# Optimization experiments

Hardware: AMD Instinct MI355X
Metric: run time of the kernel (lower is better)

The kernel has to match this reference:

```python
import jax, jax.numpy as jnp
import numpy as np

MAX_PATH_DISTANCE = 5


def setup_inputs() -> dict:
    key = jax.random.key(0)
    k1, k2, k3, k4, k5 = jax.random.split(key, 5)
    N = 8192
    E = 4_000_000
    x = jax.random.normal(k1, (N, 128), dtype=jnp.float32)
    src = jax.random.randint(k2, (E,), 0, N, dtype=jnp.int64)
    dst = jax.random.randint(k3, (E,), 0, N, dtype=jnp.int64)
    # path lengths; original computes len(paths[src][dst]) >= 1
    path_len = jax.random.randint(k4, (E,), 0, 6, dtype=jnp.int64)
    # learned parameter b of shape [max_path_distance]
    b = jax.random.normal(k5, (MAX_PATH_DISTANCE,), dtype=jnp.float32)
    return {"x": x, "b": b, "src": src, "dst": dst, "path_len": path_len}


def reference(x, b, src, dst, path_len):
    N = x.shape[0]
    # index = min(len, max_path_distance) - 1, clamped to valid range
    idx = jnp.clip(path_len, 1, MAX_PATH_DISTANCE) - 1  # [E]
    vals = b[idx]  # [E] gather from tiny table
    spatial = jnp.zeros((N, N), dtype=b.dtype)
    spatial = spatial.at[src, dst].set(vals)  # scatter into pairwise bias matrix
    return spatial
```

## Files before the change

kernel.cpp:

```cpp
#include <hip/hip_runtime.h>

#define MAX_PATH_DISTANCE 5
#define NROW 8192
#define ROWS_PER_BKT 128
#define NBKT 64
#define SLICES 17
#define EPB 4096
#define CAPB (SLICES * EPB)
#define CAPR 768
#define BLK 256
#define NWAVE 4


__device__ __forceinline__ int clamp_bidx(int pl) {
    int c = pl < 1 ? 1 : (pl > MAX_PATH_DISTANCE ? MAX_PATH_DISTANCE : pl);
    return c - 1;
}

__global__ __launch_bounds__(BLK) void se_coarse(
        const int4* __restrict__ src4, const int4* __restrict__ dst4,
        const int4* __restrict__ plen4,
        unsigned long long* __restrict__ bkt,
        unsigned int* __restrict__ bkt_cur, int E4) {
    __shared__ unsigned long long stage[EPB];
    __shared__ unsigned int hist[NWAVE][NBKT], wbase[NWAVE][NBKT];
    __shared__ unsigned int base_l[NBKT], gbase[NBKT], s_total;
    const int tid = threadIdx.x;
    const int w   = tid >> 6;
    const int q0  = blockIdx.x * (EPB / 4);

    for (int i = tid; i < NWAVE * NBKT; i += BLK)
        ((unsigned int*)hist)[i] = 0u;
    __syncthreads();

    unsigned long long ent[16];
#pragma unroll
    for (int g = 0; g < 4; ++g) {
        int q = q0 + g * BLK + tid;
        if (q < E4) {
            int4 s = src4[q], d = dst4[q], p = plen4[q];
            int ss[4] = {s.x, s.y, s.z, s.w};
            int dd[4] = {d.x, d.y, d.z, d.w};
            int pp[4] = {p.x, p.y, p.z, p.w};
#pragma unroll
            for (int c = 0; c < 4; ++c) {
                int e = q * 4 + c;
                unsigned int key = ((unsigned int)(e + 1) << 3)
                                 | (unsigned int)clamp_bidx(pp[c]);
                unsigned long long v =
                      ((unsigned long long)(unsigned int)ss[c] << 38)
                    | ((unsigned long long)(unsigned int)dd[c] << 25)
                    | (unsigned long long)key;
                ent[g * 4 + c] = v;
                atomicAdd(&hist[w][(unsigned int)(v >> 45)], 1u);
            }
        } else {
#pragma unroll
            for (int c = 0; c < 4; ++c) ent[g * 4 + c] = 0ull;
        }
    }
    __syncthreads();

    if (tid < NBKT)
        base_l[tid] = hist[0][tid] + hist[1][tid] + hist[2][tid] + hist[3][tid];
    __syncthreads();
    if (tid == 0) {
        unsigned int run = 0;
        for (int i = 0; i < NBKT; ++i) {
            unsigned int t = base_l[i]; base_l[i] = run; run += t;
        }
        s_total = run;
    }
    __syncthreads();
    if (tid < NBKT) {
        unsigned int t = base_l[tid];
        unsigned int tot = 0;
#pragma unroll
        for (int ww = 0; ww < NWAVE; ++ww) {
            wbase[ww][tid] = t; t += hist[ww][tid]; tot += hist[ww][tid];
        }
        gbase[tid] = atomicAdd(&bkt_cur[tid], tot);
    }
    __syncthreads();

#pragma unroll
    for (int j = 0; j < 16; ++j) {
        if (ent[j]) {
            unsigned int bb = (unsigned int)(ent[j] >> 45);
            unsigned int p  = atomicAdd(&wbase[w][bb], 1u);
            stage[p] = ent[j];
        }
    }
    __syncthreads();

    const unsigned int total = s_total;
    for (unsigned int i = tid; i < total; i += BLK) {
        unsigned long long v = stage[i];
        unsigned int bb  = (unsigned int)(v >> 45);
        unsigned int pos = gbase[bb] + (i - base_l[bb]);
        if (pos < CAPB) bkt[(size_t)bb * CAPB + pos] = v;
    }
}

__global__ __launch_bounds__(BLK) void se_fine(
        const unsigned long long* __restrict__ bkt,
        const unsigned int* __restrict__ bkt_cur,
        unsigned long long* __restrict__ rbins,
        unsigned int* __restrict__ rcur) {
    __shared__ unsigned long long stage[EPB];
    __shared__ unsigned int hist[NWAVE][ROWS_PER_BKT], wbase[NWAVE][ROWS_PER_BKT];
    __shared__ unsigned int base_l[ROWS_PER_BKT], gbase[ROWS_PER_BKT], s_total;
    const int tid = threadIdx.x;
    const int w   = tid >> 6;
    const int b   = blockIdx.x / SLICES;
    const int sl  = blockIdx.x % SLICES;

    unsigned int cnt = bkt_cur[b]; if (cnt > CAPB) cnt = CAPB;
    const int i0 = sl * EPB;
    int n = (int)cnt - i0;
    if (n <= 0) return;
    if (n > EPB) n = EPB;

    for (int i = tid; i < NWAVE * ROWS_PER_BKT; i += BLK)
        ((unsigned int*)hist)[i] = 0u;
    __syncthreads();

    const unsigned long long* bp = bkt + (size_t)b * CAPB + i0;
    unsigned long long ent[16];
#pragma unroll
    for (int j = 0; j < 16; ++j) {
        int i = j * BLK + tid;
        ent[j] = 0ull;
        if (i < n) {
            unsigned long long v = bp[i];
            ent[j] = v;
            atomicAdd(&hist[w][(unsigned int)(v >> 38) & 127u], 1u);
        }
    }
    __syncthreads();

    if (tid < ROWS_PER_BKT)
        base_l[tid] = hist[0][tid] + hist[1][tid] + hist[2][tid] + hist[3][tid];
    __syncthreads();
    if (tid == 0) {
        unsigned int run = 0;
        for (int i = 0; i < ROWS_PER_BKT; ++i) {
            unsigned int t = base_l[i]; base_l[i] = run; run += t;
        }
        s_total = run;
    }
    __syncthreads();
    if (tid < ROWS_PER_BKT) {
        unsigned int t = base_l[tid];
        unsigned int tot = 0;
#pragma unroll
        for (int ww = 0; ww < NWAVE; ++ww) {
            wbase[ww][tid] = t; t += hist[ww][tid]; tot += hist[ww][tid];
        }
        gbase[tid] = atomicAdd(&rcur[b * ROWS_PER_BKT + tid], tot);
    }
    __syncthreads();

#pragma unroll
    for (int j = 0; j < 16; ++j) {
        if (ent[j]) {
            unsigned int rl = (unsigned int)(ent[j] >> 38) & 127u;
            unsigned int p  = atomicAdd(&wbase[w][rl], 1u);
            stage[p] = ent[j];
        }
    }
    __syncthreads();

    const unsigned int total = s_total;
    for (unsigned int i = tid; i < total; i += BLK) {
        unsigned long long v = stage[i];
        unsigned int s   = (unsigned int)((v >> 38) & 0x1FFFu);
        unsigned int rl  = s & 127u;
        unsigned int pos = gbase[rl] + (i - base_l[rl]);
        if (pos < CAPR) rbins[(size_t)s * CAPR + pos] = v;
    }
}

__global__ __launch_bounds__(BLK) void se_rows(
        const unsigned long long* __restrict__ rbins,
        const unsigned int* __restrict__ rcur,
        const float* __restrict__ b,
        float* __restrict__ out) {
    __shared__ unsigned int lds[NROW];
    const int r = blockIdx.x, tid = threadIdx.x;

    for (int i = tid; i < NROW; i += BLK) lds[i] = 0u;

    unsigned int cnt = rcur[r]; if (cnt > CAPR) cnt = CAPR;
    const unsigned long long* bp = rbins + (size_t)r * CAPR;

    unsigned long long ev[3];
    int ne = 0;
    for (unsigned int i = tid; i < cnt; i += BLK) ev[ne++] = bp[i];
    __syncthreads();

    for (int k = 0; k < ne; ++k) {
        unsigned long long v = ev[k];
        atomicMax(&lds[(unsigned int)((v >> 25) & 0x1FFFu)],
                  (unsigned int)(v & 0x1FFFFFFu));
    }
    __syncthreads();

    for (int k = 0; k < ne; ++k) {
        unsigned long long v = ev[k];
        unsigned int key = (unsigned int)(v & 0x1FFFFFFu);
        unsigned int d   = (unsigned int)((v >> 25) & 0x1FFFu);
        if (lds[d] == key) lds[d] = __float_as_uint(b[key & 7u]);
    }
    __syncthreads();

    float4* out4 = reinterpret_cast<float4*>(out + (size_t)r * NROW);
    const float4* l4 = reinterpret_cast<const float4*>(lds);
    for (int k = tid; k < NROW / 4; k += BLK) out4[k] = l4[k];
}


__global__ void se_scatter_keys(const int* __restrict__ src,
                                const int* __restrict__ dst,
                                const int* __restrict__ plen,
                                unsigned int* __restrict__ out,
                                int E, int N) {
    int e = blockIdx.x * blockDim.x + threadIdx.x;
    if (e >= E) return;
    unsigned int key = ((unsigned int)(e + 1) << 3)
                     | (unsigned int)clamp_bidx(plen[e]);
    atomicMax(&out[(size_t)src[e] * (size_t)N + (size_t)dst[e]], key);
}

__global__ void se_resolve(const int* __restrict__ src,
                           const int* __restrict__ dst,
                           const int* __restrict__ plen,
                           const float* __restrict__ b,
                           unsigned int* __restrict__ out,
                           int E, int N) {
    int e = blockIdx.x * blockDim.x + threadIdx.x;
    if (e >= E) return;
    unsigned int key = ((unsigned int)(e + 1) << 3)
                     | (unsigned int)clamp_bidx(plen[e]);
    size_t off = (size_t)src[e] * (size_t)N + (size_t)dst[e];
    if (out[off] == key) {
        reinterpret_cast<float*>(out)[off] = b[key & 7u];
    }
}


extern "C" void kernel_launch(void* const* d_in, const int* in_sizes, int n_in,
                              void* d_out, int out_size, void* d_ws, size_t ws_size,
                              hipStream_t stream) {
    const float* b    = (const float*)d_in[1];
    const int*   src  = (const int*)d_in[2];
    const int*   dst  = (const int*)d_in[3];
    const int*   plen = (const int*)d_in[4];

    const int N = in_sizes[0] / 128;
    const int E = in_sizes[2];

    const size_t rbins_bytes = (size_t)NROW * CAPR * sizeof(unsigned long long);
    const size_t bkt_bytes   = (size_t)NBKT * CAPB * sizeof(unsigned long long);
    const size_t rcur_bytes  = (size_t)NROW * sizeof(unsigned int);
    const size_t bcur_bytes  = (size_t)NBKT * sizeof(unsigned int);
    const size_t need = rbins_bytes + bkt_bytes + rcur_bytes + bcur_bytes;

    const int block = 256;
    const int gridE = (E + block - 1) / block;

    if (N == NROW && (unsigned int)E < (1u << 22) && (E % 4) == 0 &&
        ws_size >= need) {
        unsigned long long* rbins = (unsigned long long*)d_ws;
        unsigned long long* bktp  = (unsigned long long*)((char*)d_ws + rbins_bytes);
        unsigned int* rcur  = (unsigned int*)((char*)d_ws + rbins_bytes + bkt_bytes);

        hipMemsetAsync(rcur, 0, rcur_bytes + bcur_bytes, stream);
        unsigned int* bcur = rcur + NROW;
        se_coarse<<<(E + EPB - 1) / EPB, BLK, 0, stream>>>(
            (const int4*)src, (const int4*)dst, (const int4*)plen,
            bktp, bcur, E / 4);
        se_fine<<<NBKT * SLICES, BLK, 0, stream>>>(bktp, bcur, rbins, rcur);
        se_rows<<<NROW, BLK, 0, stream>>>(rbins, rcur, b, (float*)d_out);
    } else {
        hipMemsetAsync(d_out, 0, (size_t)out_size * sizeof(float), stream);
        se_scatter_keys<<<gridE, block, 0, stream>>>(src, dst, plen,
                                                     (unsigned int*)d_out, E, N);
        se_resolve<<<gridE, block, 0, stream>>>(src, dst, plen, b,
                                                (unsigned int*)d_out, E, N);
    }
}
```

Measured before the change: 118.0 us.

## Fuse coarse, fine and row passes into one persistent cooperative kernel

Merges the memset and the three bucketing kernels into a single cooperative persistent kernel, using grid-wide syncs between phases and grid-stride task loops. The goal is to remove launch gaps and the separate memset. SLICES drops to 16 so slice indexing becomes shifts and masks, which lowers per-bucket capacity and risks overflow for skewed buckets. In exchange, occupancy is limited by the persistent grid, and grid syncs plus the occupancy/device-property queries run on every call.

```diff
diff --git a/kernel.cpp b/kernel.cpp
--- a/kernel.cpp
+++ b/kernel.cpp
@@ -1,10 +1,13 @@
 #include <hip/hip_runtime.h>
+#include <hip/hip_cooperative_groups.h>
+
+namespace cg = cooperative_groups;
 
 #define MAX_PATH_DISTANCE 5
 #define NROW 8192
 #define ROWS_PER_BKT 128
 #define NBKT 64
-#define SLICES 17
+#define SLICES 16
 #define EPB 4096
 #define CAPB (SLICES * EPB)
 #define CAPR 768
@@ -17,206 +20,206 @@
     return c - 1;
 }
 
-__global__ __launch_bounds__(BLK) void se_coarse(
+__global__ __launch_bounds__(BLK) void se_fused(
         const int4* __restrict__ src4, const int4* __restrict__ dst4,
-        const int4* __restrict__ plen4,
+        const int4* __restrict__ plen4, const float* __restrict__ b,
         unsigned long long* __restrict__ bkt,
-        unsigned int* __restrict__ bkt_cur, int E4) {
-    __shared__ unsigned long long stage[EPB];
-    __shared__ unsigned int hist[NWAVE][NBKT], wbase[NWAVE][NBKT];
-    __shared__ unsigned int base_l[NBKT], gbase[NBKT], s_total;
+        unsigned long long* __restrict__ rbins,
+        unsigned int* __restrict__ rcur,
+        float* __restrict__ out,
+        int E4, int nC) {
+    __shared__ __align__(16) unsigned long long stage[EPB];
+    __shared__ unsigned int hist[NWAVE][ROWS_PER_BKT];
+    __shared__ unsigned int wb[NWAVE][ROWS_PER_BKT];
+    __shared__ unsigned int base_l[ROWS_PER_BKT], gbase[ROWS_PER_BKT];
+    __shared__ unsigned int s_total;
+
     const int tid = threadIdx.x;
     const int w   = tid >> 6;
-    const int q0  = blockIdx.x * (EPB / 4);
-
-    for (int i = tid; i < NWAVE * NBKT; i += BLK)
-        ((unsigned int*)hist)[i] = 0u;
-    __syncthreads();
-
-    unsigned long long ent[16];
-#pragma unroll
-    for (int g = 0; g < 4; ++g) {
-        int q = q0 + g * BLK + tid;
-        if (q < E4) {
-            int4 s = src4[q], d = dst4[q], p = plen4[q];
-            int ss[4] = {s.x, s.y, s.z, s.w};
-            int dd[4] = {d.x, d.y, d.z, d.w};
-            int pp[4] = {p.x, p.y, p.z, p.w};
-#pragma unroll
-            for (int c = 0; c < 4; ++c) {
-                int e = q * 4 + c;
-                unsigned int key = ((unsigned int)(e + 1) << 3)
-                                 | (unsigned int)clamp_bidx(pp[c]);
-                unsigned long long v =
-                      ((unsigned long long)(unsigned int)ss[c] << 38)
-                    | ((unsigned long long)(unsigned int)dd[c] << 25)
-                    | (unsigned long long)key;
-                ent[g * 4 + c] = v;
-                atomicAdd(&hist[w][(unsigned int)(v >> 45)], 1u);
-            }
-        } else {
-#pragma unroll
-            for (int c = 0; c < 4; ++c) ent[g * 4 + c] = 0ull;
-        }
-    }
-    __syncthreads();
-
-    if (tid < NBKT)
-        base_l[tid] = hist[0][tid] + hist[1][tid] + hist[2][tid] + hist[3][tid];
-    __syncthreads();
-    if (tid == 0) {
-        unsigned int run = 0;
-        for (int i = 0; i < NBKT; ++i) {
-            unsigned int t = base_l[i]; base_l[i] = run; run += t;
-        }
-        s_total = run;
-    }
-    __syncthreads();
-    if (tid < NBKT) {
-        unsigned int t = base_l[tid];
-        unsigned int tot = 0;
-#pragma unroll
-        for (int ww = 0; ww < NWAVE; ++ww) {
-            wbase[ww][tid] = t; t += hist[ww][tid]; tot += hist[ww][tid];
-        }
-        gbase[tid] = atomicAdd(&bkt_cur[tid], tot);
-    }
-    __syncthreads();
-
-#pragma unroll
-    for (int j = 0; j < 16; ++j) {
-        if (ent[j]) {
-            unsigned int bb = (unsigned int)(ent[j] >> 45);
-            unsigned int p  = atomicAdd(&wbase[w][bb], 1u);
-            stage[p] = ent[j];
-        }
-    }
-    __syncthreads();
-
-    const unsigned int total = s_total;
-    for (unsigned int i = tid; i < total; i += BLK) {
-        unsigned long long v = stage[i];
-        unsigned int bb  = (unsigned int)(v >> 45);
-        unsigned int pos = gbase[bb] + (i - base_l[bb]);
-        if (pos < CAPB) bkt[(size_t)bb * CAPB + pos] = v;
-    }
-}
-
-__global__ __launch_bounds__(BLK) void se_fine(
-        const unsigned long long* __restrict__ bkt,
-        const unsigned int* __restrict__ bkt_cur,
-        unsigned long long* __restrict__ rbins,
-        unsigned int* __restrict__ rcur) {
-    __shared__ unsigned long long stage[EPB];
-    __shared__ unsigned int hist[NWAVE][ROWS_PER_BKT], wbase[NWAVE][ROWS_PER_BKT];
-    __shared__ unsigned int base_l[ROWS_PER_BKT], gbase[ROWS_PER_BKT], s_total;
-    const int tid = threadIdx.x;
-    const int w   = tid >> 6;
-    const int b   = blockIdx.x / SLICES;
-    const int sl  = blockIdx.x % SLICES;
-
-    unsigned int cnt = bkt_cur[b]; if (cnt > CAPB) cnt = CAPB;
-    const int i0 = sl * EPB;
-    int n = (int)cnt - i0;
-    if (n <= 0) return;
-    if (n > EPB) n = EPB;
-
-    for (int i = tid; i < NWAVE * ROWS_PER_BKT; i += BLK)
-        ((unsigned int*)hist)[i] = 0u;
-    __syncthreads();
-
-    const unsigned long long* bp = bkt + (size_t)b * CAPB + i0;
-    unsigned long long ent[16];
-#pragma unroll
-    for (int j = 0; j < 16; ++j) {
-        int i = j * BLK + tid;
-        ent[j] = 0ull;
-        if (i < n) {
-            unsigned long long v = bp[i];
-            ent[j] = v;
-            atomicAdd(&hist[w][(unsigned int)(v >> 38) & 127u], 1u);
-        }
-    }
-    __syncthreads();
-
-    if (tid < ROWS_PER_BKT)
-        base_l[tid] = hist[0][tid] + hist[1][tid] + hist[2][tid] + hist[3][tid];
-    __syncthreads();
-    if (tid == 0) {
-        unsigned int run = 0;
-        for (int i = 0; i < ROWS_PER_BKT; ++i) {
-            unsigned int t = base_l[i]; base_l[i] = run; run += t;
-        }
-        s_total = run;
-    }
-    __syncthreads();
-    if (tid < ROWS_PER_BKT) {
-        unsigned int t = base_l[tid];
-        unsigned int tot = 0;
-#pragma unroll
-        for (int ww = 0; ww < NWAVE; ++ww) {
-            wbase[ww][tid] = t; t += hist[ww][tid]; tot += hist[ww][tid];
-        }
-        gbase[tid] = atomicAdd(&rcur[b * ROWS_PER_BKT + tid], tot);
-    }
-    __syncthreads();
-
-#pragma unroll
-    for (int j = 0; j < 16; ++j) {
-        if (ent[j]) {
-            unsigned int rl = (unsigned int)(ent[j] >> 38) & 127u;
-            unsigned int p  = atomicAdd(&wbase[w][rl], 1u);
-            stage[p] = ent[j];
-        }
-    }
-    __syncthreads();
-
-    const unsigned int total = s_total;
-    for (unsigned int i = tid; i < total; i += BLK) {
-        unsigned long long v = stage[i];
-        unsigned int s   = (unsigned int)((v >> 38) & 0x1FFFu);
-        unsigned int rl  = s & 127u;
-        unsigned int pos = gbase[rl] + (i - base_l[rl]);
-        if (pos < CAPR) rbins[(size_t)s * CAPR + pos] = v;
-    }
-}
-
-__global__ __launch_bounds__(BLK) void se_rows(
-        const unsigned long long* __restrict__ rbins,
-        const unsigned int* __restrict__ rcur,
-        const float* __restrict__ b,
-        float* __restrict__ out) {
-    __shared__ unsigned int lds[NROW];
-    const int r = blockIdx.x, tid = threadIdx.x;
-
-    for (int i = tid; i < NROW; i += BLK) lds[i] = 0u;
-
-    unsigned int cnt = rcur[r]; if (cnt > CAPR) cnt = CAPR;
-    const unsigned long long* bp = rbins + (size_t)r * CAPR;
-
-    unsigned long long ev[3];
-    int ne = 0;
-    for (unsigned int i = tid; i < cnt; i += BLK) ev[ne++] = bp[i];
-    __syncthreads();
-
-    for (int k = 0; k < ne; ++k) {
-        unsigned long long v = ev[k];
-        atomicMax(&lds[(unsigned int)((v >> 25) & 0x1FFFu)],
-                  (unsigned int)(v & 0x1FFFFFFu));
-    }
-    __syncthreads();
-
-    for (int k = 0; k < ne; ++k) {
-        unsigned long long v = ev[k];
-        unsigned int key = (unsigned int)(v & 0x1FFFFFFu);
-        unsigned int d   = (unsigned int)((v >> 25) & 0x1FFFu);
-        if (lds[d] == key) lds[d] = __float_as_uint(b[key & 7u]);
-    }
-    __syncthreads();
-
-    float4* out4 = reinterpret_cast<float4*>(out + (size_t)r * NROW);
-    const float4* l4 = reinterpret_cast<const float4*>(lds);
-    for (int k = tid; k < NROW / 4; k += BLK) out4[k] = l4[k];
+    const int G   = gridDim.x;
+    unsigned int* bcur = rcur + NROW;
+
+    for (int i = blockIdx.x * BLK + tid; i < NROW + NBKT; i += G * BLK)
+        rcur[i] = 0u;
+    cg::this_grid().sync();
+
+    for (int task = blockIdx.x; task < nC; task += G) {
+        const int q0 = task * (EPB / 4);
+        for (int i = tid; i < NWAVE * ROWS_PER_BKT; i += BLK)
+            (&hist[0][0])[i] = 0u;
+        __syncthreads();
+
+        unsigned long long ent[16];
+#pragma unroll
+        for (int g = 0; g < 4; ++g) {
+            int q = q0 + g * BLK + tid;
+            if (q < E4) {
+                int4 s = src4[q], d = dst4[q], p = plen4[q];
+                int ss[4] = {s.x, s.y, s.z, s.w};
+                int dd[4] = {d.x, d.y, d.z, d.w};
+                int pp[4] = {p.x, p.y, p.z, p.w};
+#pragma unroll
+                for (int c = 0; c < 4; ++c) {
+                    int e = (q << 2) + c;
+                    unsigned int key = ((unsigned int)(e + 1) << 3)
+                                     | (unsigned int)clamp_bidx(pp[c]);
+                    unsigned long long v =
+                          ((unsigned long long)(unsigned int)ss[c] << 38)
+                        | ((unsigned long long)(unsigned int)dd[c] << 25)
+                        | (unsigned long long)key;
+                    ent[g * 4 + c] = v;
+                    atomicAdd(&hist[w][(unsigned int)(v >> 45)], 1u);
+                }
+            } else {
+#pragma unroll
+                for (int c = 0; c < 4; ++c) ent[g * 4 + c] = 0ull;
+            }
+        }
+        __syncthreads();
+
+        if (tid < NBKT)
+            base_l[tid] = hist[0][tid] + hist[1][tid] + hist[2][tid] + hist[3][tid];
+        __syncthreads();
+        if (tid == 0) {
+            unsigned int run = 0;
+            for (int i = 0; i < NBKT; ++i) {
+                unsigned int t = base_l[i]; base_l[i] = run; run += t;
+            }
+            s_total = run;
+        }
+        __syncthreads();
+        if (tid < NBKT) {
+            unsigned int t = base_l[tid], tot = 0;
+#pragma unroll
+            for (int ww = 0; ww < NWAVE; ++ww) {
+                wb[ww][tid] = t; t += hist[ww][tid]; tot += hist[ww][tid];
+            }
+            gbase[tid] = atomicAdd(&bcur[tid], tot);
+        }
+        __syncthreads();
+
+#pragma unroll
+        for (int j = 0; j < 16; ++j) {
+            if (ent[j]) {
+                unsigned int bb = (unsigned int)(ent[j] >> 45);
+                unsigned int p  = atomicAdd(&wb[w][bb], 1u);
+                stage[p] = ent[j];
+            }
+        }
+        __syncthreads();
+
+        const unsigned int total = s_total;
+        for (unsigned int i = tid; i < total; i += BLK) {
+            unsigned long long v = stage[i];
+            unsigned int bb  = (unsigned int)(v >> 45);
+            unsigned int pos = gbase[bb] + (i - base_l[bb]);
+            if (pos < CAPB) bkt[(size_t)bb * CAPB + pos] = v;
+        }
+        __syncthreads();
+    }
+    cg::this_grid().sync();
+
+    for (int task = blockIdx.x; task < NBKT * SLICES; task += G) {
+        const int bb = task >> 4;
+        const int sl = task & (SLICES - 1);
+        unsigned int cnt = bcur[bb]; if (cnt > CAPB) cnt = CAPB;
+        const int i0 = sl * EPB;
+        int n = (int)cnt - i0;
+        if (n > EPB) n = EPB;
+        if (n > 0) {
+            for (int i = tid; i < NWAVE * ROWS_PER_BKT; i += BLK)
+                (&hist[0][0])[i] = 0u;
+            __syncthreads();
+
+            const unsigned long long* bp = bkt + (size_t)bb * CAPB + i0;
+            unsigned long long ent[16];
+#pragma unroll
+            for (int j = 0; j < 16; ++j) {
+                int i = j * BLK + tid;
+                ent[j] = 0ull;
+                if (i < n) {
+                    ent[j] = bp[i];
+                    atomicAdd(&hist[w][(unsigned int)(ent[j] >> 38) & 127u], 1u);
+                }
+            }
+            __syncthreads();
+
+            if (tid < ROWS_PER_BKT)
+                base_l[tid] = hist[0][tid] + hist[1][tid]
+                            + hist[2][tid] + hist[3][tid];
+            __syncthreads();
+            if (tid == 0) {
+                unsigned int run = 0;
+                for (int i = 0; i < ROWS_PER_BKT; ++i) {
+                    unsigned int t = base_l[i]; base_l[i] = run; run += t;
+                }
+                s_total = run;
+            }
+            __syncthreads();
+            if (tid < ROWS_PER_BKT) {
+                unsigned int t = base_l[tid], tot = 0;
+#pragma unroll
+                for (int ww = 0; ww < NWAVE; ++ww) {
+                    wb[ww][tid] = t; t += hist[ww][tid]; tot += hist[ww][tid];
+                }
+                gbase[tid] = atomicAdd(&rcur[bb * ROWS_PER_BKT + tid], tot);
+            }
+            __syncthreads();
+
+#pragma unroll
+            for (int j = 0; j < 16; ++j) {
+                if (ent[j]) {
+                    unsigned int rl = (unsigned int)(ent[j] >> 38) & 127u;
+                    unsigned int p  = atomicAdd(&wb[w][rl], 1u);
+                    stage[p] = ent[j];
+                }
+            }
+            __syncthreads();
+
+            const unsigned int total = s_total;
+            for (unsigned int i = tid; i < total; i += BLK) {
+                unsigned long long v = stage[i];
+                unsigned int srow = (unsigned int)((v >> 38) & 0x1FFFu);
+                unsigned int rl   = srow & 127u;
+                unsigned int pos  = gbase[rl] + (i - base_l[rl]);
+                if (pos < CAPR) rbins[(size_t)srow * CAPR + pos] = v;
+            }
+            __syncthreads();
+        }
+    }
+    cg::this_grid().sync();
+
+    unsigned int* lrow = reinterpret_cast<unsigned int*>(stage);
+    for (int r = blockIdx.x; r < NROW; r += G) {
+        __syncthreads();
+        for (int i = tid; i < NROW; i += BLK) lrow[i] = 0u;
+
+        unsigned int cnt = rcur[r]; if (cnt > CAPR) cnt = CAPR;
+        const unsigned long long* bp = rbins + (size_t)r * CAPR;
+        unsigned long long ev[3];
+        int ne = 0;
+        for (unsigned int i = tid; i < cnt; i += BLK) ev[ne++] = bp[i];
+        __syncthreads();
+
+        for (int k = 0; k < ne; ++k) {
+            unsigned long long v = ev[k];
+            atomicMax(&lrow[(unsigned int)((v >> 25) & 0x1FFFu)],
+                      (unsigned int)(v & 0x1FFFFFFu));
+        }
+        __syncthreads();
+
+        for (int k = 0; k < ne; ++k) {
+            unsigned long long v = ev[k];
+            unsigned int key = (unsigned int)(v & 0x1FFFFFFu);
+            unsigned int d   = (unsigned int)((v >> 25) & 0x1FFFu);
+            if (lrow[d] == key) lrow[d] = __float_as_uint(b[key & 7u]);
+        }
+        __syncthreads();
+
+        float4* out4 = reinterpret_cast<float4*>(out + (size_t)r * NROW);
+        const float4* l4 = reinterpret_cast<const float4*>(lrow);
+        for (int k = tid; k < NROW / 4; k += BLK) out4[k] = l4[k];
+    }
 }
 
 
@@ -262,27 +265,54 @@
 
     const size_t rbins_bytes = (size_t)NROW * CAPR * sizeof(unsigned long long);
     const size_t bkt_bytes   = (size_t)NBKT * CAPB * sizeof(unsigned long long);
-    const size_t rcur_bytes  = (size_t)NROW * sizeof(unsigned int);
-    const size_t bcur_bytes  = (size_t)NBKT * sizeof(unsigned int);
-    const size_t need = rbins_bytes + bkt_bytes + rcur_bytes + bcur_bytes;
-
-    const int block = 256;
-    const int gridE = (E + block - 1) / block;
-
-    if (N == NROW && (unsigned int)E < (1u << 22) && (E % 4) == 0 &&
-        ws_size >= need) {
+    const size_t cur_bytes   = (size_t)(NROW + NBKT) * sizeof(unsigned int);
+    const size_t need = rbins_bytes + bkt_bytes + cur_bytes;
+
+    bool fast = (N == NROW) && (E > 0) && (E <= 4000000) && ((E % 4) == 0) &&
+                (ws_size >= need);
+
+    int grid = 0;
+    if (fast) {
+        int occ = 0;
+        if (hipOccupancyMaxActiveBlocksPerMultiprocessor(
+                &occ, se_fused, BLK, 0) != hipSuccess || occ <= 0) {
+            fast = false;
+        } else {
+            int devId = 0;
+            hipGetDevice(&devId);
+            hipDeviceProp_t prop;
+            if (hipGetDeviceProperties(&prop, devId) != hipSuccess) {
+                fast = false;
+            } else {
+                grid = occ * prop.multiProcessorCount;
+                if (grid > NROW) grid = NROW;
+                if (grid < 1) fast = false;
+            }
+        }
+    }
+
+    if (fast) {
         unsigned long long* rbins = (unsigned long long*)d_ws;
-        unsigned long long* bktp  = (unsigned long long*)((char*)d_ws + rbins_bytes);
-        unsigned int* rcur  = (unsigned int*)((char*)d_ws + rbins_bytes + bkt_bytes);
-
-        hipMemsetAsync(rcur, 0, rcur_bytes + bcur_bytes, stream);
-        unsigned int* bcur = rcur + NROW;
-        se_coarse<<<(E + EPB - 1) / EPB, BLK, 0, stream>>>(
-            (const int4*)src, (const int4*)dst, (const int4*)plen,
-            bktp, bcur, E / 4);
-        se_fine<<<NBKT * SLICES, BLK, 0, stream>>>(bktp, bcur, rbins, rcur);
-        se_rows<<<NROW, BLK, 0, stream>>>(rbins, rcur, b, (float*)d_out);
+        unsigned long long* bktp  =
+            (unsigned long long*)((char*)d_ws + rbins_bytes);
+        unsigned int* rcur =
+            (unsigned int*)((char*)d_ws + rbins_bytes + bkt_bytes);
+
+        const int4* src4  = (const int4*)src;
+        const int4* dst4  = (const int4*)dst;
+        const int4* plen4 = (const int4*)plen;
+        float* out = (float*)d_out;
+        int E4 = E / 4;
+        int nC = (E + EPB - 1) / EPB;
+
+        void* args[] = {(void*)&src4, (void*)&dst4, (void*)&plen4, (void*)&b,
+                        (void*)&bktp, (void*)&rbins, (void*)&rcur, (void*)&out,
+                        (void*)&E4, (void*)&nC};
+        hipLaunchCooperativeKernel((const void*)se_fused, dim3(grid), dim3(BLK),
+                                   args, 0, stream);
     } else {
+        const int block = 256;
+        const int gridE = (E + block - 1) / block;
         hipMemsetAsync(d_out, 0, (size_t)out_size * sizeof(float), stream);
         se_scatter_keys<<<gridE, block, 0, stream>>>(src, dst, plen,
                                                      (unsigned int*)d_out, E, N);
```

Result: slower. 297.4 us (+152.0%).
